# Performance work log

Hardware: AMD Instinct MI355X
Metric: run time of the kernel (lower is better)

## Reference

```python
import jax, jax.numpy as jnp
import numpy as np

N_NODES, N_EDGES, N_GRAPHS = 100000, 800000, 64
X_DIM, E_DIM, U_DIM, H = 128, 64, 128, 128
BN_EPS = 1e-5


def _bn(x, gamma, beta):
    # BatchNorm1d, training mode: biased batch stats over dim 0
    m = x.mean(axis=0)
    v = x.var(axis=0)
    return (x - m) * jax.lax.rsqrt(v + BN_EPS) * gamma + beta


def _mlp(x, Wa, ba, g, be, Wb, bb):
    h = jax.nn.selu(_bn(x @ Wa + ba, g, be))
    return h @ Wb + bb


def setup_inputs() -> dict:
    key = jax.random.key(0)
    ks = jax.random.split(key, 10)
    x = jax.random.normal(ks[0], (N_NODES, X_DIM), jnp.float32)
    edge_attr = jax.random.normal(ks[1], (N_EDGES, E_DIM), jnp.float32)
    u = jax.random.normal(ks[2], (N_GRAPHS, U_DIM), jnp.float32)
    edge_index = jax.random.randint(ks[3], (2, N_EDGES), 0, N_NODES, jnp.int32)
    batch = jnp.sort(jax.random.randint(ks[4], (N_NODES,), 0, N_GRAPHS, jnp.int32))

    def lin(k, fan_in, fan_out):
        return jax.random.normal(k, (fan_in, fan_out), jnp.float32) / np.sqrt(fan_in)

    return {
        "x": x, "edge_attr": edge_attr, "u": u,
        "W1a": lin(ks[5], X_DIM + E_DIM, H), "b1a": jnp.zeros(H),
        "g1": jnp.ones(H), "be1": jnp.zeros(H),
        "W1b": lin(ks[6], H, H), "b1b": jnp.zeros(H),
        "W2a": lin(ks[7], X_DIM + H + U_DIM, H), "b2a": jnp.zeros(H),
        "g2": jnp.ones(H), "be2": jnp.zeros(H),
        "W2b": lin(ks[8], H, H), "b2b": jnp.zeros(H),
        "edge_index": edge_index, "batch": batch,
    }


def reference(x, edge_attr, u, W1a, b1a, g1, be1, W1b, b1b,
              W2a, b2a, g2, be2, W2b, b2b, edge_index, batch):
    row, col = edge_index[0], edge_index[1]
    n = x.shape[0]
    # gather source node feats, run edge MLP
    out = jnp.concatenate([x[row], edge_attr], axis=1)        # [E, X+Ed]
    out = _mlp(out, W1a, b1a, g1, be1, W1b, b1b)              # [E, H]
    # scatter-mean over destination nodes
    s = jax.ops.segment_sum(out, col, num_segments=n)         # [N, H]
    cnt = jax.ops.segment_sum(jnp.ones((out.shape[0], 1), out.dtype), col,
                              num_segments=n)
    agg = s / jnp.maximum(cnt, 1.0)
    # node update MLP
    out2 = jnp.concatenate([x, agg, u[batch]], axis=1)        # [N, X+H+U]
    return _mlp(out2, W2a, b2a, g2, be2, W2b, b2b)
```

## Files before the change

kernel.cpp:

```cpp
#include <hip/hip_runtime.h>
#include <hip/hip_bf16.h>
#include <math.h>


typedef __attribute__((ext_vector_type(8))) short bfrag;
typedef __attribute__((ext_vector_type(4))) float f32x4;
typedef __attribute__((ext_vector_type(4))) float f4raw;

#define N_EDGES 800000
#define N_NODES 100000
#define BN_EPS 1e-5f

static __device__ __forceinline__ short f2bf(float f) {
    union { float f; unsigned u; } v; v.f = f;
    unsigned r = (v.u + 0x7FFFu + ((v.u >> 16) & 1u)) >> 16;
    return (short)r;
}
static __device__ __forceinline__ float bf2f(short h) {
    union { unsigned u; float f; } v;
    v.u = ((unsigned)(unsigned short)h) << 16;
    return v.f;
}

static __device__ __forceinline__ bfrag load8f_bf(const float* __restrict__ p) {
    float4 a = *(const float4*)p;
    float4 b = *(const float4*)(p + 4);
    bfrag r;
    r[0] = f2bf(a.x); r[1] = f2bf(a.y); r[2] = f2bf(a.z); r[3] = f2bf(a.w);
    r[4] = f2bf(b.x); r[5] = f2bf(b.y); r[6] = f2bf(b.z); r[7] = f2bf(b.w);
    return r;
}
static __device__ __forceinline__ bfrag load8f_bf_nt(const float* __restrict__ p) {
    f4raw a = __builtin_nontemporal_load((const f4raw*)p);
    f4raw b = __builtin_nontemporal_load((const f4raw*)(p + 4));
    bfrag r;
    r[0] = f2bf(a[0]); r[1] = f2bf(a[1]); r[2] = f2bf(a[2]); r[3] = f2bf(a[3]);
    r[4] = f2bf(b[0]); r[5] = f2bf(b[1]); r[6] = f2bf(b[2]); r[7] = f2bf(b[3]);
    return r;
}

static __device__ __forceinline__ float selu_f(float v) {
    return v > 0.f ? 1.0507009873554805f * v
                   : 1.7580993408473766f * (__expf(v) - 1.0f);
}

static __device__ __forceinline__ void pack_slot(short* __restrict__ Wp, int k, int n, float val) {
    int kb = k >> 5, g = (k >> 3) & 3, j = k & 7;
    Wp[(((size_t)kb * 128 + n) * 4 + g) * 8 + j] = f2bf(val);
}

__global__ void prep(const float* __restrict__ W1a, const float* __restrict__ W1b,
                     const float* __restrict__ b1b, const float* __restrict__ W2a,
                     const float* __restrict__ W2b,
                     short* __restrict__ Wp1x, short* __restrict__ Wp1e,
                     short* __restrict__ Wp2a, short* __restrict__ Wp2b,
                     float* __restrict__ cb,
                     const int* __restrict__ colI, int* __restrict__ CNTi, int E)
{
    const int b = blockIdx.x, t = threadIdx.x;
    if (b < 64) {
        int idx = b * 256 + t; int k = idx >> 7, n = idx & 127;
        pack_slot(Wp1x, k, n, W1a[idx]);
    } else if (b < 96) {
        int idx = (b - 64) * 256 + t; int k = idx >> 7, n = idx & 127;
        pack_slot(Wp1e, k, n, W1a[128 * 128 + idx]);
    } else if (b < 160) {
        int idx = (b - 96) * 256 + t; int k = idx >> 7, n = idx & 127;
        pack_slot(Wp2a, k, n, W2a[idx]);
    } else if (b < 224) {
        int k = (b - 160) * 2 + (t >> 7);
        int n = t & 127;
        int kt = ((k & 7) << 4) + (k >> 3);
        float s = 0.f;
        for (int j = 0; j < 128; ++j)
            s += W1b[kt * 128 + j] * W2a[(size_t)(128 + j) * 128 + n];
        pack_slot(Wp2a + 16384, k, n, s);
    } else if (b < 288) {
        int idx = (b - 224) * 256 + t; int k = idx >> 7, n = idx & 127;
        pack_slot(Wp2a + 32768, k, n, W2a[(size_t)256 * 128 + idx]);
    } else if (b < 352) {
        int idx = (b - 288) * 256 + t; int k = idx >> 7, n = idx & 127;
        int kt = ((k & 7) << 4) + (k >> 3);
        pack_slot(Wp2b, k, n, W2b[(size_t)kt * 128 + n]);
    } else if (b == 352) {
        if (t < 128) {
            float s = 0.f;
            for (int j = 0; j < 128; ++j) s += b1b[j] * W2a[(size_t)(128 + j) * 128 + t];
            cb[t] = s;
        }
    } else {
        int e = (b - 353) * 256 + t;
        if (e < E) atomicAdd(&CNTi[colI[e]], 1);
    }
}

__global__ __launch_bounds__(1024) void scanF(const int* __restrict__ cnt,
                                              int* __restrict__ off, int N) {
    __shared__ int ls[1024];
    const int b = blockIdx.x, tid = threadIdx.x;
    int s = 0;
    const int lim = b * 1024;
    for (int i = tid; i < lim; i += 1024) s += cnt[i];
    ls[tid] = s;
    __syncthreads();
    for (int d = 512; d > 0; d >>= 1) {
        if (tid < d) ls[tid] += ls[tid + d];
        __syncthreads();
    }
    const int base = ls[0];
    __syncthreads();
    const int i = lim + tid;
    int v = (i < N) ? cnt[i] : 0;
    ls[tid] = v;
    __syncthreads();
    for (int d = 1; d < 1024; d <<= 1) {
        int t = (tid >= d) ? ls[tid - d] : 0;
        __syncthreads();
        ls[tid] += t;
        __syncthreads();
    }
    if (i < N) off[i] = base + ls[tid] - v;
}

__global__ void fill_k(const int* __restrict__ col, int* __restrict__ off,
                       int* __restrict__ spos, float* __restrict__ statsz, int E) {
    if (blockIdx.x == gridDim.x - 1) {
        statsz[threadIdx.x] = 0.f;
        statsz[256 + threadIdx.x] = 0.f;
        return;
    }
    int e = blockIdx.x * 256 + threadIdx.x;
    if (e < E) spos[e] = atomicAdd(&off[col[e]], 1);
}

__global__ __launch_bounds__(256) void gemmX(
    const float* __restrict__ x, const short* __restrict__ Wp,
    short* __restrict__ Xap, int N)
{
    const int lane = threadIdx.x & 63, wave = threadIdx.x >> 6;
    const int m0 = blockIdx.x * 128 + wave * 32;
    if (m0 >= N) return;
    const int lr = lane & 15, lg = lane >> 4;
    const int v0 = m0 + lr, v1 = m0 + 16 + lr;

    f32x4 acc[2][8];
#pragma unroll
    for (int t = 0; t < 2; ++t)
#pragma unroll
        for (int n = 0; n < 8; ++n) acc[t][n] = (f32x4){0.f, 0.f, 0.f, 0.f};

#pragma unroll
    for (int kb = 0; kb < 4; ++kb) {
        bfrag a0 = load8f_bf(x + (size_t)v0 * 128 + kb * 32 + lg * 8);
        bfrag a1 = load8f_bf(x + (size_t)v1 * 128 + kb * 32 + lg * 8);
        const short* wb = Wp + (size_t)kb * 4096;
#pragma unroll
        for (int n0 = 0; n0 < 8; ++n0) {
            bfrag b = *(const bfrag*)(wb + ((n0 * 16 + lr) * 4 + lg) * 8);
            acc[0][n0] = __builtin_amdgcn_mfma_f32_16x16x32_bf16(a0, b, acc[0][n0], 0, 0, 0);
            acc[1][n0] = __builtin_amdgcn_mfma_f32_16x16x32_bf16(a1, b, acc[1][n0], 0, 0, 0);
        }
    }
#pragma unroll
    for (int t = 0; t < 2; ++t) {
        const int rbase = m0 + t * 16 + lg * 4;
#pragma unroll
        for (int r = 0; r < 4; ++r) {
            bfrag o;
#pragma unroll
            for (int n0 = 0; n0 < 8; ++n0) o[n0] = f2bf(acc[t][n0][r]);
            *(bfrag*)(Xap + (size_t)(rbase + r) * 128 + lr * 8) = o;
        }
    }
}

__global__ __launch_bounds__(256) void gemm1n(
    const float* __restrict__ ea, const int* __restrict__ rowI,
    const int* __restrict__ SPOS, const short* __restrict__ Wp,
    const short* __restrict__ Xap, short* __restrict__ T1p,
    float* __restrict__ stats, int E)
{
    const int lane = threadIdx.x & 63, wave = threadIdx.x >> 6;
    const int lr = lane & 15, lg = lane >> 4;

    float ps[8], qs[8];
#pragma unroll
    for (int n0 = 0; n0 < 8; ++n0) { ps[n0] = 0.f; qs[n0] = 0.f; }

    const int NT = E >> 7;
    for (int tile = blockIdx.x; tile < NT; tile += gridDim.x) {
        const int m0 = tile * 128 + wave * 32;

        int spos[2][4];
        bfrag xa[2][4];
#pragma unroll
        for (int t = 0; t < 2; ++t) {
            const int rbase = m0 + t * 16 + lg * 4;
#pragma unroll
            for (int r = 0; r < 4; ++r) {
                const int e = rbase + r;
                spos[t][r] = SPOS[e];
                xa[t][r] = *(const bfrag*)(Xap + (size_t)rowI[e] * 128 + lr * 8);
            }
        }

        const float* er0 = ea + (size_t)(m0 + lr) * 64;
        const float* er1 = ea + (size_t)(m0 + 16 + lr) * 64;

        f32x4 acc[2][8];
#pragma unroll
        for (int t = 0; t < 2; ++t)
#pragma unroll
            for (int n = 0; n < 8; ++n) acc[t][n] = (f32x4){0.f, 0.f, 0.f, 0.f};

#pragma unroll
        for (int kb = 0; kb < 2; ++kb) {
            bfrag a0 = load8f_bf_nt(er0 + kb * 32 + lg * 8);
            bfrag a1 = load8f_bf_nt(er1 + kb * 32 + lg * 8);
            const short* wb = Wp + (size_t)kb * 4096;
#pragma unroll
            for (int n0 = 0; n0 < 8; ++n0) {
                bfrag b = *(const bfrag*)(wb + ((n0 * 16 + lr) * 4 + lg) * 8);
                acc[0][n0] = __builtin_amdgcn_mfma_f32_16x16x32_bf16(a0, b, acc[0][n0], 0, 0, 0);
                acc[1][n0] = __builtin_amdgcn_mfma_f32_16x16x32_bf16(a1, b, acc[1][n0], 0, 0, 0);
            }
        }

#pragma unroll
        for (int t = 0; t < 2; ++t) {
#pragma unroll
            for (int r = 0; r < 4; ++r) {
                bfrag o;
#pragma unroll
                for (int n0 = 0; n0 < 8; ++n0) {
                    float v = acc[t][n0][r] + bf2f(xa[t][r][n0]);
                    ps[n0] += v; qs[n0] += v * v;
                    o[n0] = f2bf(v);
                }
                *(bfrag*)(T1p + (size_t)spos[t][r] * 128 + lr * 8) = o;
            }
        }
    }

    __shared__ float ls[256];
    ls[threadIdx.x] = 0.f;
    __syncthreads();
#pragma unroll
    for (int n0 = 0; n0 < 8; ++n0) {
        const int c = n0 * 16 + lr;
        float p = ps[n0], q = qs[n0];
        p += __shfl_xor(p, 16); p += __shfl_xor(p, 32);
        q += __shfl_xor(q, 16); q += __shfl_xor(q, 32);
        if (lg == 0) { atomicAdd(&ls[c], p); atomicAdd(&ls[128 + c], q); }
    }
    __syncthreads();
    atomicAdd(&stats[threadIdx.x], ls[threadIdx.x]);
}

__global__ __launch_bounds__(256) void segsel(
    const short* __restrict__ T1p, const float* __restrict__ stats,
    const float* __restrict__ g1, const float* __restrict__ be1,
    const int* __restrict__ OFF, const int* __restrict__ CNTi,
    short* __restrict__ Aggm, int N, float invR)
{
    __shared__ float ls_sc[128], ls_sh[128];
    if (threadIdx.x < 128) {
        int p = threadIdx.x;
        int c = ((p & 7) << 4) + (p >> 3);
        float mean = stats[c] * invR;
        float var = stats[128 + c] * invR - mean * mean;
        float sc = g1[c] * rsqrtf(var + BN_EPS);
        ls_sc[p] = sc;
        ls_sh[p] = be1[c] - mean * sc;
    }
    __syncthreads();

    const int lane = threadIdx.x & 63;
    const int q = lane & 15, rp = lane >> 4;
    const int wid = blockIdx.x * 4 + (threadIdx.x >> 6);
    const int nw = gridDim.x * 4;
    const int chunk = (N + nw - 1) / nw;
    const int v0 = wid * chunk;
    const int v1 = (v0 + chunk < N) ? v0 + chunk : N;

    float sc8[8], sh8[8];
#pragma unroll
    for (int i = 0; i < 8; ++i) { sc8[i] = ls_sc[q * 8 + i]; sh8[i] = ls_sh[q * 8 + i]; }

    for (int v = v0; v < v1; ++v) {
        const int cnt = CNTi[v];
        const int beg = OFF[v] - cnt;
        const short* base = T1p + (size_t)beg * 128 + q * 8;
        float a[8];
#pragma unroll
        for (int i = 0; i < 8; ++i) a[i] = 0.f;
        int j = 0;
        for (; j + 8 <= cnt; j += 8) {
            bfrag w0 = *(const bfrag*)(base + (size_t)(j + rp) * 128);
            bfrag w1 = *(const bfrag*)(base + (size_t)(j + 4 + rp) * 128);
#pragma unroll
            for (int i = 0; i < 8; ++i) {
                a[i] += selu_f(sc8[i] * bf2f(w0[i]) + sh8[i]);
                a[i] += selu_f(sc8[i] * bf2f(w1[i]) + sh8[i]);
            }
        }
        for (; j + 4 <= cnt; j += 4) {
            bfrag w = *(const bfrag*)(base + (size_t)(j + rp) * 128);
#pragma unroll
            for (int i = 0; i < 8; ++i) a[i] += selu_f(sc8[i] * bf2f(w[i]) + sh8[i]);
        }
        if (j + rp < cnt) {
            bfrag w = *(const bfrag*)(base + (size_t)(j + rp) * 128);
#pragma unroll
            for (int i = 0; i < 8; ++i) a[i] += selu_f(sc8[i] * bf2f(w[i]) + sh8[i]);
        }
#pragma unroll
        for (int i = 0; i < 8; ++i) {
            a[i] += __shfl_xor(a[i], 16);
            a[i] += __shfl_xor(a[i], 32);
        }
        if (rp == 0) {
            const float inv = 1.0f / fmaxf((float)cnt, 1.0f);
            bfrag o;
#pragma unroll
            for (int i = 0; i < 8; ++i) o[i] = f2bf(a[i] * inv);
            *(bfrag*)(Aggm + (size_t)v * 128 + q * 8) = o;
        }
    }
}

__global__ __launch_bounds__(256) void gemm3_node(
    const float* __restrict__ x, const short* __restrict__ Aggm,
    const float* __restrict__ u, const int* __restrict__ batch,
    const int* __restrict__ CNTi, const float* __restrict__ cb,
    const short* __restrict__ Wp, short* __restrict__ T2p,
    float* __restrict__ stats, int N)
{
    const int lane = threadIdx.x & 63, wave = threadIdx.x >> 6;
    const int m0 = blockIdx.x * 128 + wave * 32;
    const bool active = (m0 < N);
    const int lr = lane & 15, lg = lane >> 4;
    __shared__ float ls[256];
    ls[threadIdx.x] = 0.f;
    __syncthreads();

    if (active) {
        const int v0 = m0 + lr, v1 = m0 + 16 + lr;
        const float* u0 = u + (size_t)batch[v0] * 128;
        const float* u1 = u + (size_t)batch[v1] * 128;

        f32x4 acc[2][8];
#pragma unroll
        for (int t = 0; t < 2; ++t)
#pragma unroll
            for (int n = 0; n < 8; ++n) acc[t][n] = (f32x4){0.f, 0.f, 0.f, 0.f};

#pragma unroll
        for (int kb = 0; kb < 12; ++kb) {
            bfrag a0, a1;
            if (kb >= 4 && kb < 8) {
                a0 = *(const bfrag*)(Aggm + (size_t)v0 * 128 + (kb - 4) * 32 + lg * 8);
                a1 = *(const bfrag*)(Aggm + (size_t)v1 * 128 + (kb - 4) * 32 + lg * 8);
            } else {
                const float *p0, *p1;
                if (kb < 4) {
                    p0 = x + (size_t)v0 * 128 + kb * 32 + lg * 8;
                    p1 = x + (size_t)v1 * 128 + kb * 32 + lg * 8;
                } else {
                    p0 = u0 + (kb - 8) * 32 + lg * 8;
                    p1 = u1 + (kb - 8) * 32 + lg * 8;
                }
                a0 = load8f_bf(p0);
                a1 = load8f_bf(p1);
            }
            const short* wb = Wp + (size_t)kb * 4096;
#pragma unroll
            for (int n0 = 0; n0 < 8; ++n0) {
                bfrag b = *(const bfrag*)(wb + ((n0 * 16 + lr) * 4 + lg) * 8);
                acc[0][n0] = __builtin_amdgcn_mfma_f32_16x16x32_bf16(a0, b, acc[0][n0], 0, 0, 0);
                acc[1][n0] = __builtin_amdgcn_mfma_f32_16x16x32_bf16(a1, b, acc[1][n0], 0, 0, 0);
            }
        }
        float cbl[8];
#pragma unroll
        for (int n0 = 0; n0 < 8; ++n0) cbl[n0] = cb[n0 * 16 + lr];
        float ps[8], qs[8];
#pragma unroll
        for (int n0 = 0; n0 < 8; ++n0) { ps[n0] = 0.f; qs[n0] = 0.f; }
#pragma unroll
        for (int t = 0; t < 2; ++t) {
            const int rbase = m0 + t * 16 + lg * 4;
            float fl[4];
#pragma unroll
            for (int r = 0; r < 4; ++r) fl[r] = (CNTi[rbase + r] > 0) ? 1.f : 0.f;
#pragma unroll
            for (int r = 0; r < 4; ++r) {
                bfrag o;
#pragma unroll
                for (int n0 = 0; n0 < 8; ++n0) {
                    float v = acc[t][n0][r] + fl[r] * cbl[n0];
                    ps[n0] += v; qs[n0] += v * v;
                    o[n0] = f2bf(v);
                }
                *(bfrag*)(T2p + (size_t)(rbase + r) * 128 + lr * 8) = o;
            }
        }
#pragma unroll
        for (int n0 = 0; n0 < 8; ++n0) {
            const int c = n0 * 16 + lr;
            float p = ps[n0], q = qs[n0];
            p += __shfl_xor(p, 16); p += __shfl_xor(p, 32);
            q += __shfl_xor(q, 16); q += __shfl_xor(q, 32);
            if (lg == 0) { atomicAdd(&ls[c], p); atomicAdd(&ls[128 + c], q); }
        }
    }
    __syncthreads();
    atomicAdd(&stats[threadIdx.x], ls[threadIdx.x]);
}

__global__ __launch_bounds__(256) void gemm4_node(
    const short* __restrict__ T2p, const float* __restrict__ stats,
    const float* __restrict__ g2, const float* __restrict__ be2,
    const short* __restrict__ Wp, const float* __restrict__ b2b,
    float* __restrict__ out, int N, float invR)
{
    __shared__ float ls_sc[128], ls_sh[128];
    if (threadIdx.x < 128) {
        int c = threadIdx.x;
        float mean = stats[c] * invR;
        float var = stats[128 + c] * invR - mean * mean;
        float sc = g2[c] * rsqrtf(var + BN_EPS);
        ls_sc[c] = sc;
        ls_sh[c] = be2[c] - mean * sc;
    }
    __syncthreads();

    const int lane = threadIdx.x & 63, wave = threadIdx.x >> 6;
    const int m0 = blockIdx.x * 128 + wave * 32;
    if (m0 >= N) return;
    const int lr = lane & 15, lg = lane >> 4;
    const int e0 = m0 + lr, e1 = m0 + 16 + lr;

    f32x4 acc[2][8];
#pragma unroll
    for (int n0 = 0; n0 < 8; ++n0) {
        float bias = b2b[n0 * 16 + lr];
        acc[0][n0] = (f32x4){bias, bias, bias, bias};
        acc[1][n0] = (f32x4){bias, bias, bias, bias};
    }
#pragma unroll
    for (int kb = 0; kb < 4; ++kb) {
        float scl[8], shf[8];
#pragma unroll
        for (int j = 0; j < 8; ++j) {
            int c = j * 16 + kb * 4 + lg;
            scl[j] = ls_sc[c];
            shf[j] = ls_sh[c];
        }
        bfrag r0 = *(const bfrag*)(T2p + (size_t)e0 * 128 + kb * 32 + lg * 8);
        bfrag r1 = *(const bfrag*)(T2p + (size_t)e1 * 128 + kb * 32 + lg * 8);
        bfrag a0, a1;
#pragma unroll
        for (int j = 0; j < 8; ++j) {
            a0[j] = f2bf(selu_f(bf2f(r0[j]) * scl[j] + shf[j]));
            a1[j] = f2bf(selu_f(bf2f(r1[j]) * scl[j] + shf[j]));
        }
        const short* wb = Wp + (size_t)kb * 4096;
#pragma unroll
        for (int n0 = 0; n0 < 8; ++n0) {
            bfrag b = *(const bfrag*)(wb + ((n0 * 16 + lr) * 4 + lg) * 8);
            acc[0][n0] = __builtin_amdgcn_mfma_f32_16x16x32_bf16(a0, b, acc[0][n0], 0, 0, 0);
            acc[1][n0] = __builtin_amdgcn_mfma_f32_16x16x32_bf16(a1, b, acc[1][n0], 0, 0, 0);
        }
    }
#pragma unroll
    for (int t = 0; t < 2; ++t) {
        const int rbase = m0 + t * 16 + lg * 4;
#pragma unroll
        for (int n0 = 0; n0 < 8; ++n0) {
            const int c = n0 * 16 + lr;
#pragma unroll
            for (int r = 0; r < 4; ++r)
                __builtin_nontemporal_store(acc[t][n0][r],
                    out + (size_t)(rbase + r) * 128 + c);
        }
    }
}

extern "C" void kernel_launch(void* const* d_in, const int* in_sizes, int n_in,
                              void* d_out, int out_size, void* d_ws, size_t ws_size,
                              hipStream_t stream)
{
    const float* x   = (const float*)d_in[0];
    const float* ea  = (const float*)d_in[1];
    const float* u   = (const float*)d_in[2];
    const float* W1a = (const float*)d_in[3];
    const float* g1  = (const float*)d_in[5];
    const float* be1 = (const float*)d_in[6];
    const float* W1b = (const float*)d_in[7];
    const float* b1b = (const float*)d_in[8];
    const float* W2a = (const float*)d_in[9];
    const float* g2  = (const float*)d_in[11];
    const float* be2 = (const float*)d_in[12];
    const float* W2b = (const float*)d_in[13];
    const float* b2b = (const float*)d_in[14];
    const int* ei    = (const int*)d_in[15];
    const int* rowI  = ei;
    const int* colI  = ei + N_EDGES;
    const int* batch = (const int*)d_in[16];
    float* out = (float*)d_out;

    if (ws_size < 260252416ull) return;

    char* ws = (char*)d_ws;
    short* Wp1x   = (short*)(ws + 0);
    short* Wp1e   = (short*)(ws + 32768);
    short* Wp2a   = (short*)(ws + 49152);
    short* Wp2b   = (short*)(ws + 147456);
    float* cb     = (float*)(ws + 245760);
    float* stats1 = (float*)(ws + 246272);
    float* stats2 = (float*)(ws + 247296);
    int*   CNTi   = (int*)(ws + 250368);
    int*   OFF    = (int*)(ws + 650368);
    int*   SPOS   = (int*)(ws + 1052416);
    short* Aggm   = (short*)(ws + 4252416);
    short* Xap    = (short*)(ws + 29852416ull);
    short* T2p    = (short*)(ws + 29852416ull);
    short* T1p    = (short*)(ws + 55452416ull);

    hipMemsetAsync(CNTi, 0, 400000, stream);

    prep<<<353 + (N_EDGES + 255) / 256, 256, 0, stream>>>(
        W1a, W1b, b1b, W2a, W2b, Wp1x, Wp1e, Wp2a, Wp2b, cb, colI, CNTi, N_EDGES);

    scanF<<<98, 1024, 0, stream>>>(CNTi, OFF, N_NODES);
    fill_k<<<(N_EDGES + 255) / 256 + 1, 256, 0, stream>>>(colI, OFF, SPOS, stats1, N_EDGES);

    gemmX<<<(N_NODES + 127) / 128, 256, 0, stream>>>(x, Wp1x, Xap, N_NODES);

    gemm1n<<<2048, 256, 0, stream>>>(ea, rowI, SPOS, Wp1e, Xap, T1p, stats1, N_EDGES);

    segsel<<<2048, 256, 0, stream>>>(T1p, stats1, g1, be1, OFF, CNTi, Aggm,
                                     N_NODES, 1.0f / (float)N_EDGES);

    gemm3_node<<<(N_NODES + 127) / 128, 256, 0, stream>>>(x, Aggm, u, batch, CNTi, cb,
                                                          Wp2a, T2p, stats2, N_NODES);
    gemm4_node<<<(N_NODES + 127) / 128, 256, 0, stream>>>(T2p, stats2, g2, be2, Wp2b, b2b,
                                                          out, N_NODES, 1.0f / (float)N_NODES);
}
```

Measured before the change: 382.7 us.

## Store edge pre-BN intermediate in fp8 and widen segment reduction lanes

```diff
diff --git a/kernel.cpp b/kernel.cpp
--- a/kernel.cpp
+++ b/kernel.cpp
@@ -6,6 +6,8 @@
 typedef __attribute__((ext_vector_type(8))) short bfrag;
 typedef __attribute__((ext_vector_type(4))) float f32x4;
 typedef __attribute__((ext_vector_type(4))) float f4raw;
+typedef __attribute__((ext_vector_type(2))) unsigned u32x2;
+typedef __attribute__((ext_vector_type(4))) unsigned u32x4;
 
 #define N_EDGES 800000
 #define N_NODES 100000
@@ -177,7 +179,7 @@
 __global__ __launch_bounds__(256) void gemm1n(
     const float* __restrict__ ea, const int* __restrict__ rowI,
     const int* __restrict__ SPOS, const short* __restrict__ Wp,
-    const short* __restrict__ Xap, short* __restrict__ T1p,
+    const short* __restrict__ Xap, unsigned char* __restrict__ T1q,
     float* __restrict__ stats, int E)
 {
     const int lane = threadIdx.x & 63, wave = threadIdx.x >> 6;
@@ -230,14 +232,19 @@
         for (int t = 0; t < 2; ++t) {
 #pragma unroll
             for (int r = 0; r < 4; ++r) {
-                bfrag o;
+                float v[8];
 #pragma unroll
                 for (int n0 = 0; n0 < 8; ++n0) {
-                    float v = acc[t][n0][r] + bf2f(xa[t][r][n0]);
-                    ps[n0] += v; qs[n0] += v * v;
-                    o[n0] = f2bf(v);
+                    v[n0] = acc[t][n0][r] + bf2f(xa[t][r][n0]);
+                    ps[n0] += v[n0]; qs[n0] += v[n0] * v[n0];
                 }
-                *(bfrag*)(T1p + (size_t)spos[t][r] * 128 + lr * 8) = o;
+                unsigned w0 = 0, w1 = 0;
+                w0 = __builtin_amdgcn_cvt_pk_fp8_f32(v[0], v[1], w0, false);
+                w0 = __builtin_amdgcn_cvt_pk_fp8_f32(v[2], v[3], w0, true);
+                w1 = __builtin_amdgcn_cvt_pk_fp8_f32(v[4], v[5], w1, false);
+                w1 = __builtin_amdgcn_cvt_pk_fp8_f32(v[6], v[7], w1, true);
+                u32x2 o; o[0] = w0; o[1] = w1;
+                *(u32x2*)(T1q + (size_t)spos[t][r] * 128 + lr * 8) = o;
             }
         }
     }
@@ -258,7 +265,7 @@
 }
 
 __global__ __launch_bounds__(256) void segsel(
-    const short* __restrict__ T1p, const float* __restrict__ stats,
+    const unsigned char* __restrict__ T1q, const float* __restrict__ stats,
     const float* __restrict__ g1, const float* __restrict__ be1,
     const int* __restrict__ OFF, const int* __restrict__ CNTi,
     short* __restrict__ Aggm, int N, float invR)
@@ -276,55 +283,61 @@
     __syncthreads();
 
     const int lane = threadIdx.x & 63;
-    const int q = lane & 15, rp = lane >> 4;
+    const int q = lane & 7, rp = lane >> 3;
     const int wid = blockIdx.x * 4 + (threadIdx.x >> 6);
     const int nw = gridDim.x * 4;
     const int chunk = (N + nw - 1) / nw;
     const int v0 = wid * chunk;
     const int v1 = (v0 + chunk < N) ? v0 + chunk : N;
 
-    float sc8[8], sh8[8];
-#pragma unroll
-    for (int i = 0; i < 8; ++i) { sc8[i] = ls_sc[q * 8 + i]; sh8[i] = ls_sh[q * 8 + i]; }
+    float sc16[16], sh16[16];
+#pragma unroll
+    for (int i = 0; i < 16; ++i) { sc16[i] = ls_sc[q * 16 + i]; sh16[i] = ls_sh[q * 16 + i]; }
 
     for (int v = v0; v < v1; ++v) {
         const int cnt = CNTi[v];
         const int beg = OFF[v] - cnt;
-        const short* base = T1p + (size_t)beg * 128 + q * 8;
-        float a[8];
-#pragma unroll
-        for (int i = 0; i < 8; ++i) a[i] = 0.f;
+        const unsigned char* base = T1q + (size_t)beg * 128 + q * 16;
+        float a[16];
+#pragma unroll
+        for (int i = 0; i < 16; ++i) a[i] = 0.f;
         int j = 0;
         for (; j + 8 <= cnt; j += 8) {
-            bfrag w0 = *(const bfrag*)(base + (size_t)(j + rp) * 128);
-            bfrag w1 = *(const bfrag*)(base + (size_t)(j + 4 + rp) * 128);
-#pragma unroll
-            for (int i = 0; i < 8; ++i) {
-                a[i] += selu_f(sc8[i] * bf2f(w0[i]) + sh8[i]);
-                a[i] += selu_f(sc8[i] * bf2f(w1[i]) + sh8[i]);
-            }
-        }
-        for (; j + 4 <= cnt; j += 4) {
-            bfrag w = *(const bfrag*)(base + (size_t)(j + rp) * 128);
-#pragma unroll
-            for (int i = 0; i < 8; ++i) a[i] += selu_f(sc8[i] * bf2f(w[i]) + sh8[i]);
+            u32x4 w = *(const u32x4*)(base + (size_t)(j + rp) * 128);
+#pragma unroll
+            for (int wi = 0; wi < 4; ++wi) {
+                a[wi * 4 + 0] += selu_f(sc16[wi * 4 + 0] * __builtin_amdgcn_cvt_f32_fp8(w[wi], 0) + sh16[wi * 4 + 0]);
+                a[wi * 4 + 1] += selu_f(sc16[wi * 4 + 1] * __builtin_amdgcn_cvt_f32_fp8(w[wi], 1) + sh16[wi * 4 + 1]);
+                a[wi * 4 + 2] += selu_f(sc16[wi * 4 + 2] * __builtin_amdgcn_cvt_f32_fp8(w[wi], 2) + sh16[wi * 4 + 2]);
+                a[wi * 4 + 3] += selu_f(sc16[wi * 4 + 3] * __builtin_amdgcn_cvt_f32_fp8(w[wi], 3) + sh16[wi * 4 + 3]);
+            }
         }
         if (j + rp < cnt) {
-            bfrag w = *(const bfrag*)(base + (size_t)(j + rp) * 128);
-#pragma unroll
-            for (int i = 0; i < 8; ++i) a[i] += selu_f(sc8[i] * bf2f(w[i]) + sh8[i]);
-        }
-#pragma unroll
-        for (int i = 0; i < 8; ++i) {
+            u32x4 w = *(const u32x4*)(base + (size_t)(j + rp) * 128);
+#pragma unroll
+            for (int wi = 0; wi < 4; ++wi) {
+                a[wi * 4 + 0] += selu_f(sc16[wi * 4 + 0] * __builtin_amdgcn_cvt_f32_fp8(w[wi], 0) + sh16[wi * 4 + 0]);
+                a[wi * 4 + 1] += selu_f(sc16[wi * 4 + 1] * __builtin_amdgcn_cvt_f32_fp8(w[wi], 1) + sh16[wi * 4 + 1]);
+                a[wi * 4 + 2] += selu_f(sc16[wi * 4 + 2] * __builtin_amdgcn_cvt_f32_fp8(w[wi], 2) + sh16[wi * 4 + 2]);
+                a[wi * 4 + 3] += selu_f(sc16[wi * 4 + 3] * __builtin_amdgcn_cvt_f32_fp8(w[wi], 3) + sh16[wi * 4 + 3]);
+            }
+        }
+#pragma unroll
+        for (int i = 0; i < 16; ++i) {
+            a[i] += __shfl_xor(a[i], 8);
             a[i] += __shfl_xor(a[i], 16);
             a[i] += __shfl_xor(a[i], 32);
         }
         if (rp == 0) {
             const float inv = 1.0f / fmaxf((float)cnt, 1.0f);
-            bfrag o;
-#pragma unroll
-            for (int i = 0; i < 8; ++i) o[i] = f2bf(a[i] * inv);
-            *(bfrag*)(Aggm + (size_t)v * 128 + q * 8) = o;
+            bfrag o0, o1;
+#pragma unroll
+            for (int i = 0; i < 8; ++i) {
+                o0[i] = f2bf(a[i] * inv);
+                o1[i] = f2bf(a[8 + i] * inv);
+            }
+            *(bfrag*)(Aggm + (size_t)v * 128 + q * 16) = o0;
+            *(bfrag*)(Aggm + (size_t)v * 128 + q * 16 + 8) = o1;
         }
     }
 }
@@ -510,7 +523,7 @@
     const int* batch = (const int*)d_in[16];
     float* out = (float*)d_out;
 
-    if (ws_size < 260252416ull) return;
+    if (ws_size < 157852416ull) return;
 
     char* ws = (char*)d_ws;
     short* Wp1x   = (short*)(ws + 0);
@@ -526,7 +539,7 @@
     short* Aggm   = (short*)(ws + 4252416);
     short* Xap    = (short*)(ws + 29852416ull);
     short* T2p    = (short*)(ws + 29852416ull);
-    short* T1p    = (short*)(ws + 55452416ull);
+    unsigned char* T1q = (unsigned char*)(ws + 55452416ull);
 
     hipMemsetAsync(CNTi, 0, 400000, stream);
 
@@ -538,9 +551,9 @@
 
     gemmX<<<(N_NODES + 127) / 128, 256, 0, stream>>>(x, Wp1x, Xap, N_NODES);
 
-    gemm1n<<<2048, 256, 0, stream>>>(ea, rowI, SPOS, Wp1e, Xap, T1p, stats1, N_EDGES);
-
-    segsel<<<2048, 256, 0, stream>>>(T1p, stats1, g1, be1, OFF, CNTi, Aggm,
+    gemm1n<<<2048, 256, 0, stream>>>(ea, rowI, SPOS, Wp1e, Xap, T1q, stats1, N_EDGES);
+
+    segsel<<<2048, 256, 0, stream>>>(T1q, stats1, g1, be1, OFF, CNTi, Aggm,
                                      N_NODES, 1.0f / (float)N_EDGES);
 
     gemm3_node<<<(N_NODES + 127) / 128, 256, 0, stream>>>(x, Aggm, u, batch, CNTi, cb,
```

Result: slower. 453.9 us (+18.6%).
